# Performance work log

Measured on AMD Instinct MI355X. Metric: run time of the kernel, lower is better.

Reference implementation:

```python
import jax, jax.numpy as jnp
import numpy as np

DIM = 1024
NUM_HEADS = 16
HEAD_DIM = DIM // NUM_HEADS
SCALE = HEAD_DIM ** -0.5


def setup_inputs() -> dict:
    key = jax.random.key(0)
    ks = jax.random.split(key, 9)
    s = 0.02
    return {
        "x": jax.random.normal(ks[0], (4, 2048, DIM), dtype=jnp.float32),
        "Wq": jax.random.normal(ks[1], (DIM, DIM), dtype=jnp.float32) * s,
        "bq": jax.random.normal(ks[2], (DIM,), dtype=jnp.float32) * s,
        "Wk": jax.random.normal(ks[3], (DIM, DIM), dtype=jnp.float32) * s,
        "bk": jax.random.normal(ks[4], (DIM,), dtype=jnp.float32) * s,
        "Wv": jax.random.normal(ks[5], (DIM, DIM), dtype=jnp.float32) * s,
        "bv": jax.random.normal(ks[6], (DIM,), dtype=jnp.float32) * s,
        "Wo": jax.random.normal(ks[7], (DIM, DIM), dtype=jnp.float32) * s,
        "bo": jax.random.normal(ks[8], (DIM,), dtype=jnp.float32) * s,
    }


def reference(x, Wq, bq, Wk, bk, Wv, bv, Wo, bo):
    B, S, D = x.shape
    H, Dh = NUM_HEADS, HEAD_DIM

    def heads(t):  # [B,S,D] -> [B,H,S,Dh]
        return t.reshape(B, S, H, Dh).transpose(0, 2, 1, 3)

    q = heads(x @ Wq.T + bq)
    k = heads(x @ Wk.T + bk)
    v = heads(x @ Wv.T + bv)

    attn = jnp.einsum('bnqd,bnkd->bnqk', q, k) * SCALE
    attn = jax.nn.softmax(attn, axis=-1)
    out = jnp.einsum('bnqk,bnkd->bnqd', attn, v)  # [B,H,S,Dh]
    out = out.transpose(0, 2, 1, 3).reshape(B, S, D)
    return out @ Wo.T + bo
```

## Files before the change

### kernel.cpp

```cpp
#include <hip/hip_runtime.h>
#include <stdint.h>

#define DIMD 1024
#define NH   16
#define DH   64
#define BB   4
#define SS   2048
#define MTOT 8192

static constexpr float QSCALE = 0.18033688011112042f;

typedef unsigned short u16;
typedef __attribute__((ext_vector_type(8))) short bf8;
typedef __attribute__((ext_vector_type(4))) float f4;
typedef __attribute__((ext_vector_type(16))) float f16v;

#if __has_builtin(__builtin_amdgcn_exp2f)
#define EXP2(x) __builtin_amdgcn_exp2f(x)
#else
#define EXP2(x) exp2f(x)
#endif

__device__ inline u16 f2bf(float f) {
    union { float f; uint32_t u; } v; v.f = f;
    uint32_t r = v.u + 0x7fffu + ((v.u >> 16) & 1u);
    return (u16)(r >> 16);
}

__device__ inline void gld16(const void* g, void* l) {
    __builtin_amdgcn_global_load_lds(
        (const __attribute__((address_space(1))) uint32_t*)g,
        (__attribute__((address_space(3))) uint32_t*)l, 16, 0, 0);
}

__device__ inline uint32_t cvtpk(float lo, float hi) {
    uint32_t r;
    asm("v_cvt_pk_bf16_f32 %0, %1, %2" : "=v"(r) : "v"(lo), "v"(hi));
    return r;
}

__global__ void cvt_bf16(const float* __restrict__ src, u16* __restrict__ dst, int n) {
    int i = (blockIdx.x * blockDim.x + threadIdx.x) * 4;
    if (i >= n) return;
    float4 v = *(const float4*)(src + i);
    ushort4 o;
    o.x = f2bf(v.x); o.y = f2bf(v.y); o.z = f2bf(v.z); o.w = f2bf(v.w);
    *(ushort4*)(dst + i) = o;
}

__global__ __launch_bounds__(256, 2) void gemm_qkv(
    const u16* __restrict__ xb, const u16* __restrict__ Wb,
    const float* __restrict__ bq, const float* __restrict__ bk, const float* __restrict__ bv,
    u16* __restrict__ qkv, u16* __restrict__ vtb)
{
    __shared__ u16 lA[128 * 64];
    __shared__ u16 lB[128 * 64];
    const int tid = threadIdx.x;
    const int bm = blockIdx.x, bn = blockIdx.y, z = blockIdx.z;
    const u16* W = Wb + (size_t)z * DIMD * DIMD;
    const float* bias = (z == 0) ? bq : ((z == 1) ? bk : bv);
    u16* outp = qkv + (size_t)z * (size_t)MTOT * DIMD;

    const int lane = tid & 63, w = tid >> 6;
    const int wr = (w >> 1) * 64, wc = (w & 1) * 64;
    f4 acc[4][4] = {};

    const char* Abase = (const char*)xb + (size_t)(bm * 128) * 2048;
    const char* Bbase = (const char*)W + (size_t)(bn * 128) * 2048;

    for (int kt = 0; kt < 16; ++kt) {
        __syncthreads();
        #pragma unroll
        for (int p = 0; p < 4; ++p) {
            int off = (p * 256 + tid) * 16;
            int row = off >> 7, cb = off & 127;
            int scb = cb ^ ((row & 7) << 4);
            gld16(Abase + (size_t)row * 2048 + kt * 128 + scb, (char*)lA + off);
            gld16(Bbase + (size_t)row * 2048 + kt * 128 + scb, (char*)lB + off);
        }
        __syncthreads();
        #pragma unroll
        for (int ks = 0; ks < 2; ++ks) {
            const int cb = ks * 64 + ((lane >> 4) << 4);
            bf8 af[4], bfr[4];
            #pragma unroll
            for (int mi = 0; mi < 4; ++mi) {
                int r = wr + mi * 16 + (lane & 15);
                af[mi] = *(const bf8*)((const char*)lA + r * 128 + (cb ^ ((r & 7) << 4)));
            }
            #pragma unroll
            for (int ni = 0; ni < 4; ++ni) {
                int r = wc + ni * 16 + (lane & 15);
                bfr[ni] = *(const bf8*)((const char*)lB + r * 128 + (cb ^ ((r & 7) << 4)));
            }
            #pragma unroll
            for (int mi = 0; mi < 4; ++mi)
                #pragma unroll
                for (int ni = 0; ni < 4; ++ni)
                    acc[mi][ni] = __builtin_amdgcn_mfma_f32_16x16x32_bf16(af[mi], bfr[ni], acc[mi][ni], 0, 0, 0);
        }
    }

    if (z == 2) {
        #pragma unroll
        for (int ni = 0; ni < 4; ++ni) {
            int col = bn * 128 + wc + ni * 16 + (lane & 15);
            float bi = bias[col];
            int h = col >> 6, dh = col & 63;
            #pragma unroll
            for (int mi = 0; mi < 4; ++mi) {
                int row0 = bm * 128 + wr + mi * 16 + ((lane >> 4) << 2);
                int b = row0 >> 11, s = row0 & 2047;
                ushort4 st;
                st.x = f2bf(acc[mi][ni][0] + bi);
                st.y = f2bf(acc[mi][ni][1] + bi);
                st.z = f2bf(acc[mi][ni][2] + bi);
                st.w = f2bf(acc[mi][ni][3] + bi);
                *(ushort4*)(vtb + ((size_t)(b * NH + h) * DH + dh) * SS + s) = st;
            }
        }
    } else {
        const float mulv = (z == 0) ? QSCALE : 1.0f;
        #pragma unroll
        for (int ni = 0; ni < 4; ++ni) {
            int col = bn * 128 + wc + ni * 16 + (lane & 15);
            float bi = bias[col];
            int h = col >> 6, dh = col & 63;
            #pragma unroll
            for (int mi = 0; mi < 4; ++mi) {
                #pragma unroll
                for (int r = 0; r < 4; ++r) {
                    int row = bm * 128 + wr + mi * 16 + ((lane >> 4) << 2) + r;
                    int b = row >> 11, s = row & 2047;
                    outp[(((size_t)(b * NH + h) * SS + s) << 6) + dh] = f2bf((acc[mi][ni][r] + bi) * mulv);
                }
            }
        }
    }
}

__global__ __launch_bounds__(256, 2) void gemm_out(
    const u16* __restrict__ Ab, const u16* __restrict__ Wo,
    const float* __restrict__ bo, float* __restrict__ dout)
{
    __shared__ u16 lA[128 * 64];
    __shared__ u16 lB[128 * 64];
    const int tid = threadIdx.x;
    const int bm = blockIdx.x, bn = blockIdx.y;
    const int lane = tid & 63, w = tid >> 6;
    const int wr = (w >> 1) * 64, wc = (w & 1) * 64;
    f4 acc[4][4] = {};
    const char* Abase = (const char*)Ab + (size_t)(bm * 128) * 2048;
    const char* Bbase = (const char*)Wo + (size_t)(bn * 128) * 2048;

    for (int kt = 0; kt < 16; ++kt) {
        __syncthreads();
        #pragma unroll
        for (int p = 0; p < 4; ++p) {
            int off = (p * 256 + tid) * 16;
            int row = off >> 7, cb = off & 127;
            int scb = cb ^ ((row & 7) << 4);
            gld16(Abase + (size_t)row * 2048 + kt * 128 + scb, (char*)lA + off);
            gld16(Bbase + (size_t)row * 2048 + kt * 128 + scb, (char*)lB + off);
        }
        __syncthreads();
        #pragma unroll
        for (int ks = 0; ks < 2; ++ks) {
            const int cb = ks * 64 + ((lane >> 4) << 4);
            bf8 af[4], bfr[4];
            #pragma unroll
            for (int mi = 0; mi < 4; ++mi) {
                int r = wr + mi * 16 + (lane & 15);
                af[mi] = *(const bf8*)((const char*)lA + r * 128 + (cb ^ ((r & 7) << 4)));
            }
            #pragma unroll
            for (int ni = 0; ni < 4; ++ni) {
                int r = wc + ni * 16 + (lane & 15);
                bfr[ni] = *(const bf8*)((const char*)lB + r * 128 + (cb ^ ((r & 7) << 4)));
            }
            #pragma unroll
            for (int mi = 0; mi < 4; ++mi)
                #pragma unroll
                for (int ni = 0; ni < 4; ++ni)
                    acc[mi][ni] = __builtin_amdgcn_mfma_f32_16x16x32_bf16(af[mi], bfr[ni], acc[mi][ni], 0, 0, 0);
        }
    }
    #pragma unroll
    for (int ni = 0; ni < 4; ++ni) {
        int col = bn * 128 + wc + ni * 16 + (lane & 15);
        float bi = bo[col];
        #pragma unroll
        for (int mi = 0; mi < 4; ++mi) {
            #pragma unroll
            for (int r = 0; r < 4; ++r) {
                int row = bm * 128 + wr + mi * 16 + ((lane >> 4) << 2) + r;
                dout[(size_t)row * DIMD + col] = acc[mi][ni][r] + bi;
            }
        }
    }
}

__global__ __launch_bounds__(512, 2) void attn_fwd(
    const u16* __restrict__ Q, const u16* __restrict__ K,
    const u16* __restrict__ Vt, u16* __restrict__ O)
{
    __shared__ u16 lK[2][64 * 64];
    __shared__ u16 lV[2][64 * 64];

    const int tid = threadIdx.x;
    const int lane = tid & 63, w = tid >> 6;
    const int hi = lane >> 5, l31 = lane & 31;
    const int bh = blockIdx.y;
    const int qb0 = blockIdx.x * 256;
    const char* Kbase = (const char*)(K + (size_t)bh * SS * DH);
    const char* Vbase = (const char*)(Vt + (size_t)bh * DH * SS);

    const int qrow = qb0 + w * 32 + l31;
    const u16* Qp = Q + (size_t)bh * SS * DH + (size_t)qrow * DH;
    bf8 qf[4];
    #pragma unroll
    for (int kd = 0; kd < 4; ++kd)
        qf[kd] = *(const bf8*)(Qp + kd * 16 + hi * 8);

    f16v oacc0 = {}, oacc1 = {};
    float lsum = 0.f;

    auto stage = [&](int buf, int kv0) {
        int off = tid * 16;
        int row = off >> 7, cb = off & 127;
        int scb = cb ^ ((row & 7) << 4);
        gld16(Kbase + (size_t)(kv0 + row) * 128 + scb, (char*)lK[buf] + off);
        gld16(Vbase + (size_t)row * (SS * 2) + (size_t)kv0 * 2 + scb, (char*)lV[buf] + off);
    };

    stage(0, 0);
    __syncthreads();

    for (int it = 0; it < SS / 64; ++it) {
        const int cur = it & 1;
        if (it + 1 < SS / 64) stage(cur ^ 1, (it + 1) * 64);

        const char* lKc = (const char*)lK[cur];
        const char* lVc = (const char*)lV[cur];

        f16v s0 = {}, s1 = {};
        __builtin_amdgcn_s_setprio(1);
        #pragma unroll
        for (int kd = 0; kd < 4; ++kd) {
            const int colb = 32 * kd + 16 * hi;
            const int r0 = l31, r1 = 32 + l31;
            bf8 kf0 = *(const bf8*)(lKc + r0 * 128 + (colb ^ ((r0 & 7) << 4)));
            bf8 kf1 = *(const bf8*)(lKc + r1 * 128 + (colb ^ ((r1 & 7) << 4)));
            s0 = __builtin_amdgcn_mfma_f32_32x32x16_bf16(kf0, qf[kd], s0, 0, 0, 0);
            s1 = __builtin_amdgcn_mfma_f32_32x32x16_bf16(kf1, qf[kd], s1, 0, 0, 0);
        }
        __builtin_amdgcn_s_setprio(0);

        float ps[16];
        #pragma unroll
        for (int i = 0; i < 16; ++i) {
            float e0 = EXP2(s0[i]);
            float e1 = EXP2(s1[i]);
            s0[i] = e0; s1[i] = e1;
            ps[i] = e0 + e1;
        }
        float t0 = (ps[0] + ps[1]) + (ps[2] + ps[3]);
        float t1 = (ps[4] + ps[5]) + (ps[6] + ps[7]);
        float t2 = (ps[8] + ps[9]) + (ps[10] + ps[11]);
        float t3 = (ps[12] + ps[13]) + (ps[14] + ps[15]);
        lsum += (t0 + t1) + (t2 + t3);

        uint32_t wv0[8], wv1[8];
        #pragma unroll
        for (int a = 0; a < 4; ++a) {
            wv0[a * 2 + 0] = cvtpk(s0[4 * a + 0], s0[4 * a + 1]);
            wv0[a * 2 + 1] = cvtpk(s0[4 * a + 2], s0[4 * a + 3]);
            wv1[a * 2 + 0] = cvtpk(s1[4 * a + 0], s1[4 * a + 1]);
            wv1[a * 2 + 1] = cvtpk(s1[4 * a + 2], s1[4 * a + 3]);
        }

        #pragma unroll
        for (int ks = 0; ks < 4; ++ks) {
            const int kss = ks & 1;
            const uint32_t* wv = (ks < 2) ? wv0 : wv1;
            uint32_t w0 = wv[(2 * kss) * 2 + 0];
            uint32_t w1 = wv[(2 * kss) * 2 + 1];
            uint32_t w2 = wv[(2 * kss + 1) * 2 + 0];
            uint32_t w3 = wv[(2 * kss + 1) * 2 + 1];
            asm("v_permlane32_swap_b32 %0, %1" : "+v"(w0), "+v"(w2));
            asm("v_permlane32_swap_b32 %0, %1" : "+v"(w1), "+v"(w3));
            union { uint32_t u[4]; bf8 v; } pb;
            pb.u[0] = w0; pb.u[1] = w1; pb.u[2] = w2; pb.u[3] = w3;

            const int colb = 32 * ks + 16 * hi;
            const int r0 = l31, r1 = 32 + l31;
            bf8 vf0 = *(const bf8*)(lVc + r0 * 128 + (colb ^ ((r0 & 7) << 4)));
            bf8 vf1 = *(const bf8*)(lVc + r1 * 128 + (colb ^ ((r1 & 7) << 4)));
            __builtin_amdgcn_s_setprio(1);
            oacc0 = __builtin_amdgcn_mfma_f32_32x32x16_bf16(vf0, pb.v, oacc0, 0, 0, 0);
            oacc1 = __builtin_amdgcn_mfma_f32_32x32x16_bf16(vf1, pb.v, oacc1, 0, 0, 0);
            __builtin_amdgcn_s_setprio(0);
        }

        __syncthreads();
    }

    const float l = lsum + __shfl_xor(lsum, 32, 64);
    const int b = bh >> 4, h = bh & 15;
    const float inv = 1.f / l;
    u16* orow = O + (((size_t)(b * SS + qrow)) << 10) + h * DH;
    #pragma unroll
    for (int g = 0; g < 4; ++g) {
        ushort4 st0, st1;
        st0.x = f2bf(oacc0[4 * g + 0] * inv); st0.y = f2bf(oacc0[4 * g + 1] * inv);
        st0.z = f2bf(oacc0[4 * g + 2] * inv); st0.w = f2bf(oacc0[4 * g + 3] * inv);
        st1.x = f2bf(oacc1[4 * g + 0] * inv); st1.y = f2bf(oacc1[4 * g + 1] * inv);
        st1.z = f2bf(oacc1[4 * g + 2] * inv); st1.w = f2bf(oacc1[4 * g + 3] * inv);
        *(ushort4*)(orow + 8 * g + 4 * hi) = st0;
        *(ushort4*)(orow + 32 + 8 * g + 4 * hi) = st1;
    }
}

extern "C" void kernel_launch(void* const* d_in, const int* in_sizes, int n_in,
                              void* d_out, int out_size, void* d_ws, size_t ws_size,
                              hipStream_t stream) {
    const float* x  = (const float*)d_in[0];
    const float* Wq = (const float*)d_in[1];
    const float* bq = (const float*)d_in[2];
    const float* Wk = (const float*)d_in[3];
    const float* bk = (const float*)d_in[4];
    const float* Wv = (const float*)d_in[5];
    const float* bv = (const float*)d_in[6];
    const float* Wo = (const float*)d_in[7];
    const float* bo = (const float*)d_in[8];
    float* out = (float*)d_out;

    u16* wsp = (u16*)d_ws;
    const size_t NX = (size_t)MTOT * DIMD;
    const size_t NW = (size_t)DIMD * DIMD;
    u16* xb   = wsp;
    u16* Wb   = wsp + NX;
    u16* Qb   = wsp + NX + 4 * NW;
    u16* Kb   = Qb + NX;
    u16* Vtb  = Kb + NX;
    u16* attn = xb;

    cvt_bf16<<<dim3((int)(NX / 4 / 256)), 256, 0, stream>>>(x, xb, (int)NX);
    cvt_bf16<<<dim3((int)(NW / 4 / 256)), 256, 0, stream>>>(Wq, Wb + 0 * NW, (int)NW);
    cvt_bf16<<<dim3((int)(NW / 4 / 256)), 256, 0, stream>>>(Wk, Wb + 1 * NW, (int)NW);
    cvt_bf16<<<dim3((int)(NW / 4 / 256)), 256, 0, stream>>>(Wv, Wb + 2 * NW, (int)NW);
    cvt_bf16<<<dim3((int)(NW / 4 / 256)), 256, 0, stream>>>(Wo, Wb + 3 * NW, (int)NW);

    gemm_qkv<<<dim3(MTOT / 128, DIMD / 128, 3), 256, 0, stream>>>(xb, Wb, bq, bk, bv, Qb, Vtb);
    attn_fwd<<<dim3(SS / 256, BB * NH), 512, 0, stream>>>(Qb, Kb, Vtb, attn);
    gemm_out<<<dim3(MTOT / 128, DIMD / 128), 256, 0, stream>>>(attn, Wb + 3 * NW, bo, out);
}
```

Measured before the change: 185.7 us.

## Software-pipeline attention loop so PV of previous tile overlaps QK and softmax

Restructures the flash-attention inner loop so each iteration issues QK^T for tile t, then PV for tile t-1, then the softmax for tile t. This lets MFMA work overlap the exp and pack latency. V gets a triple-buffered LDS ring so a tile's V stays resident one extra iteration, and the P fragments are carried across iterations in registers. Launch bounds raise the occupancy hint from 2 to 4 blocks per CU, which tightens the register budget and risks spills given the extra live P state.

```diff
diff --git a/kernel.cpp b/kernel.cpp
--- a/kernel.cpp
+++ b/kernel.cpp
@@ -200,12 +200,12 @@
     }
 }
 
-__global__ __launch_bounds__(512, 2) void attn_fwd(
+__global__ __launch_bounds__(512, 4) void attn_fwd(
     const u16* __restrict__ Q, const u16* __restrict__ K,
     const u16* __restrict__ Vt, u16* __restrict__ O)
 {
-    __shared__ u16 lK[2][64 * 64];
-    __shared__ u16 lV[2][64 * 64];
+    __shared__ __align__(16) u16 lK[2][64 * 64];
+    __shared__ __align__(16) u16 lV[3][64 * 64];
 
     const int tid = threadIdx.x;
     const int lane = tid & 63, w = tid >> 6;
@@ -224,38 +224,46 @@
 
     f16v oacc0 = {}, oacc1 = {};
     float lsum = 0.f;
-
-    auto stage = [&](int buf, int kv0) {
+    bf8 pbv[4];
+
+    const int rswz = (l31 & 7) << 4;
+
+    auto stage = [&](int t, int vbuf) {
         int off = tid * 16;
         int row = off >> 7, cb = off & 127;
         int scb = cb ^ ((row & 7) << 4);
-        gld16(Kbase + (size_t)(kv0 + row) * 128 + scb, (char*)lK[buf] + off);
-        gld16(Vbase + (size_t)row * (SS * 2) + (size_t)kv0 * 2 + scb, (char*)lV[buf] + off);
+        int kv0 = t * 64;
+        gld16(Kbase + (size_t)(kv0 + row) * 128 + scb, (char*)lK[t & 1] + off);
+        gld16(Vbase + (size_t)row * (SS * 2) + (size_t)kv0 * 2 + scb, (char*)lV[vbuf] + off);
     };
 
-    stage(0, 0);
-    __syncthreads();
-
-    for (int it = 0; it < SS / 64; ++it) {
-        const int cur = it & 1;
-        if (it + 1 < SS / 64) stage(cur ^ 1, (it + 1) * 64);
-
-        const char* lKc = (const char*)lK[cur];
-        const char* lVc = (const char*)lV[cur];
-
-        f16v s0 = {}, s1 = {};
+    auto QKfn = [&](const char* lKc, f16v& s0, f16v& s1) {
         __builtin_amdgcn_s_setprio(1);
         #pragma unroll
         for (int kd = 0; kd < 4; ++kd) {
             const int colb = 32 * kd + 16 * hi;
-            const int r0 = l31, r1 = 32 + l31;
-            bf8 kf0 = *(const bf8*)(lKc + r0 * 128 + (colb ^ ((r0 & 7) << 4)));
-            bf8 kf1 = *(const bf8*)(lKc + r1 * 128 + (colb ^ ((r1 & 7) << 4)));
+            bf8 kf0 = *(const bf8*)(lKc + l31 * 128 + (colb ^ rswz));
+            bf8 kf1 = *(const bf8*)(lKc + (32 + l31) * 128 + (colb ^ rswz));
             s0 = __builtin_amdgcn_mfma_f32_32x32x16_bf16(kf0, qf[kd], s0, 0, 0, 0);
             s1 = __builtin_amdgcn_mfma_f32_32x32x16_bf16(kf1, qf[kd], s1, 0, 0, 0);
         }
         __builtin_amdgcn_s_setprio(0);
-
+    };
+
+    auto PVfn = [&](const char* lVc) {
+        __builtin_amdgcn_s_setprio(1);
+        #pragma unroll
+        for (int ks = 0; ks < 4; ++ks) {
+            const int colb = 32 * ks + 16 * hi;
+            bf8 vf0 = *(const bf8*)(lVc + l31 * 128 + (colb ^ rswz));
+            bf8 vf1 = *(const bf8*)(lVc + (32 + l31) * 128 + (colb ^ rswz));
+            oacc0 = __builtin_amdgcn_mfma_f32_32x32x16_bf16(vf0, pbv[ks], oacc0, 0, 0, 0);
+            oacc1 = __builtin_amdgcn_mfma_f32_32x32x16_bf16(vf1, pbv[ks], oacc1, 0, 0, 0);
+        }
+        __builtin_amdgcn_s_setprio(0);
+    };
+
+    auto SMfn = [&](f16v& s0, f16v& s1) {
         float ps[16];
         #pragma unroll
         for (int i = 0; i < 16; ++i) {
@@ -278,32 +286,44 @@
             wv1[a * 2 + 0] = cvtpk(s1[4 * a + 0], s1[4 * a + 1]);
             wv1[a * 2 + 1] = cvtpk(s1[4 * a + 2], s1[4 * a + 3]);
         }
-
         #pragma unroll
         for (int ks = 0; ks < 4; ++ks) {
             const int kss = ks & 1;
-            const uint32_t* wv = (ks < 2) ? wv0 : wv1;
-            uint32_t w0 = wv[(2 * kss) * 2 + 0];
-            uint32_t w1 = wv[(2 * kss) * 2 + 1];
-            uint32_t w2 = wv[(2 * kss + 1) * 2 + 0];
-            uint32_t w3 = wv[(2 * kss + 1) * 2 + 1];
+            uint32_t w0 = (ks < 2) ? wv0[4 * kss + 0] : wv1[4 * kss + 0];
+            uint32_t w1 = (ks < 2) ? wv0[4 * kss + 1] : wv1[4 * kss + 1];
+            uint32_t w2 = (ks < 2) ? wv0[4 * kss + 2] : wv1[4 * kss + 2];
+            uint32_t w3 = (ks < 2) ? wv0[4 * kss + 3] : wv1[4 * kss + 3];
             asm("v_permlane32_swap_b32 %0, %1" : "+v"(w0), "+v"(w2));
             asm("v_permlane32_swap_b32 %0, %1" : "+v"(w1), "+v"(w3));
             union { uint32_t u[4]; bf8 v; } pb;
             pb.u[0] = w0; pb.u[1] = w1; pb.u[2] = w2; pb.u[3] = w3;
-
-            const int colb = 32 * ks + 16 * hi;
-            const int r0 = l31, r1 = 32 + l31;
-            bf8 vf0 = *(const bf8*)(lVc + r0 * 128 + (colb ^ ((r0 & 7) << 4)));
-            bf8 vf1 = *(const bf8*)(lVc + r1 * 128 + (colb ^ ((r1 & 7) << 4)));
-            __builtin_amdgcn_s_setprio(1);
-            oacc0 = __builtin_amdgcn_mfma_f32_32x32x16_bf16(vf0, pb.v, oacc0, 0, 0, 0);
-            oacc1 = __builtin_amdgcn_mfma_f32_32x32x16_bf16(vf1, pb.v, oacc1, 0, 0, 0);
-            __builtin_amdgcn_s_setprio(0);
-        }
-
-        __syncthreads();
-    }
+            pbv[ks] = pb.v;
+        }
+    };
+
+    stage(0, 0);
+    __syncthreads();
+    {
+        stage(1, 1);
+        f16v s0 = {}, s1 = {};
+        QKfn((const char*)lK[0], s0, s1);
+        SMfn(s0, s1);
+        __syncthreads();
+    }
+
+    int vW = 2;
+    int vR = 0;
+    for (int t = 1; t < SS / 64; ++t) {
+        if (t + 1 < SS / 64) stage(t + 1, vW);
+        f16v s0 = {}, s1 = {};
+        QKfn((const char*)lK[t & 1], s0, s1);
+        PVfn((const char*)lV[vR]);
+        SMfn(s0, s1);
+        __syncthreads();
+        vW = (vW == 2) ? 0 : vW + 1;
+        vR = (vR == 2) ? 0 : vR + 1;
+    }
+    PVfn((const char*)lV[vR]);
 
     const float l = lsum + __shfl_xor(lsum, 32, 64);
     const int b = bh >> 4, h = bh & 15;
```

Result: no change. 183.4 us (-1.3%).
